# Kernel tuning notes

Hardware: AMD Instinct MI355X
Metric: run time of the kernel (lower is better)

Reference implementation:

```python
import jax, jax.numpy as jnp
import numpy as np

L, B, T, SA, ST = 6, 32, 256, 512, 128
D, H, HD, DFF, OUT = 1024, 16, 64, 4096, 3
ROPE_THETA = 10000.0

def setup_inputs() -> dict:
    key = jax.random.key(0)
    ks = jax.random.split(key, 24)
    w = lambda k, shape: jax.random.normal(k, shape, jnp.float32) * 0.02
    inp = {
        'x':    jax.random.normal(ks[0], (B, T, D), jnp.float32),
        'cond': jax.random.normal(ks[1], (B, D), jnp.float32),
        'adp':  jax.random.normal(ks[2], (B, SA, D), jnp.float32),
        'task': jax.random.normal(ks[3], (B, ST, D), jnp.float32),
        'Wq':  w(ks[4], (L, D, D)),  'bq': jnp.zeros((L, D)),
        'Wks': w(ks[5], (L, D, D)),  'Wvs': w(ks[6], (L, D, D)),
        'Wka': w(ks[7], (L, D, D)),  'Wva': w(ks[8], (L, D, D)),
        'Wkt': w(ks[9], (L, D, D)),  'Wvt': w(ks[10], (L, D, D)),
        'Wo':  w(ks[11], (L, D, D)), 'bo': jnp.zeros((L, D)),
        'qnw': jnp.ones((L, HD)),    'knw': jnp.ones((L, HD)),
        'gate': jnp.zeros((L,)),
        'Wada': w(ks[12], (L, D, 6 * D)), 'bada': jnp.zeros((L, 6 * D)),
        'W1': w(ks[13], (L, D, DFF)), 'b1': jnp.zeros((L, DFF)),
        'W2': w(ks[14], (L, DFF, D)), 'b2': jnp.zeros((L, D)),
        'lnf_w': jnp.ones((D,)), 'lnf_b': jnp.zeros((D,)),
        'Wout': w(ks[15], (D, OUT)), 'bout': jnp.zeros((OUT,)),
    }
    return inp

def _ln(x, eps=1e-5):
    m = x.mean(-1, keepdims=True)
    v = ((x - m) ** 2).mean(-1, keepdims=True)
    return (x - m) * jax.lax.rsqrt(v + eps)

def _rms(x, wgt, eps=1e-6):
    return x * jax.lax.rsqrt((x * x).mean(-1, keepdims=True) + eps) * wgt

def _rotate_half(x):
    h = x.shape[-1] // 2
    return jnp.concatenate([-x[..., h:], x[..., :h]], axis=-1)

def _rope(x, cos, sin):
    # x: (B,S,H,HD); cos/sin: (S,1,HD)
    return x * cos + _rotate_half(x) * sin

def _cos_sin(S):
    inv = 1.0 / (ROPE_THETA ** (jnp.arange(0, HD, 2, dtype=jnp.float32) / HD))
    f = jnp.arange(S, dtype=jnp.float32)[:, None] * inv[None, :]
    emb = jnp.concatenate([f, f], axis=-1)  # (S, HD)
    return jnp.cos(emb)[:, None, :], jnp.sin(emb)[:, None, :]

def _forward(x, cond, adp, task, Wq, bq, Wks, Wvs, Wka, Wva, Wkt, Wvt, Wo, bo,
             qnw, knw, gate, Wada, bada, W1, b1, W2, b2, lnf_w, lnf_b, Wout, bout):
    cosT, sinT = _cos_sin(T)
    cosA, sinA = _cos_sin(SA)
    cosK, sinK = _cos_sin(ST)
    scale = 1.0 / jnp.sqrt(jnp.float32(HD))
    heads = lambda t, W: (t @ W).reshape(t.shape[0], t.shape[1], H, HD)
    for i in range(L):
        ada = jax.nn.silu(cond) @ Wada[i] + bada[i]
        s1, sc1, g1, s2, sc2, g2 = jnp.split(ada, 6, axis=-1)  # each (B,D)
        h = _ln(x) * (1.0 + sc1[:, None]) + s1[:, None]
        # self source: RoPE on Q and K; cross sources: RoPE on K only
        q = _rope(_rms(heads(h, Wq[i]) + bq[i].reshape(H, HD), qnw[i]), cosT, sinT)
        k_s = _rope(_rms(heads(h, Wks[i]), knw[i]), cosT, sinT)
        v_s = heads(h, Wvs[i])
        k_a = _rope(_rms(heads(adp, Wka[i]), knw[i]), cosA, sinA)
        v_a = heads(adp, Wva[i])
        k_t = _rope(_rms(heads(task, Wkt[i]), knw[i]), cosK, sinK)
        v_t = heads(task, Wvt[i])
        ss = jnp.einsum('bthd,bshd->bhts', q, k_s) * scale
        sa = jnp.einsum('bthd,bshd->bhts', q, k_a) * scale
        st = jnp.einsum('bthd,bshd->bhts', q, k_t) * scale * jax.nn.sigmoid(gate[i])
        attn = jax.nn.softmax(jnp.concatenate([ss, sa, st], axis=-1), axis=-1)
        v = jnp.concatenate([v_s, v_a, v_t], axis=1)  # (B, T+SA+ST, H, HD)
        o = jnp.einsum('bhts,bshd->bthd', attn, v).reshape(x.shape[0], T, D)
        x = x + g1[:, None] * (o @ Wo[i] + bo[i])
        h2 = _ln(x) * (1.0 + sc2[:, None]) + s2[:, None]
        ff = jax.nn.gelu(h2 @ W1[i] + b1[i]) @ W2[i] + b2[i]
        x = x + g2[:, None] * ff
    y = _ln(x) * lnf_w + lnf_b
    return y @ Wout + bout

def reference(x, cond, adp, task, Wq, bq, Wks, Wvs, Wka, Wva, Wkt, Wvt, Wo, bo,
              qnw, knw, gate, Wada, bada, W1, b1, W2, b2, lnf_w, lnf_b, Wout, bout):
    return _forward(x, cond, adp, task, Wq, bq, Wks, Wvs, Wka, Wva, Wkt, Wvt, Wo, bo,
                    qnw, knw, gate, Wada, bada, W1, b1, W2, b2, lnf_w, lnf_b, Wout, bout)
```

## Files before the change

kernel.cpp:

```cpp
#include <hip/hip_runtime.h>
#include <stdint.h>

#define DEV static __device__ __forceinline__

#define BB 32
#define TT 256
#define SAA 512
#define STT 128
#define DD 1024
#define HH 16
#define HDD 64
#define DFFF 4096
#define SS 896
#define LL 6

using bf16x8 = __attribute__((ext_vector_type(8))) short;
using f32x4  = __attribute__((ext_vector_type(4))) float;

DEV uint16_t f2bf(float f){
  uint32_t u = __float_as_uint(f);
  uint32_t r = (u + 0x7fffu + ((u >> 16) & 1u)) >> 16;
  return (uint16_t)r;
}
DEV float bf2f(uint16_t b){ return __uint_as_float(((uint32_t)b) << 16); }

typedef __attribute__((address_space(3))) void lds_vt;
typedef __attribute__((address_space(1))) void glb_vt;

DEV void gl_lds16(const uint16_t* g, uint16_t* l){
  __builtin_amdgcn_global_load_lds((const glb_vt*)g, (lds_vt*)l, 16, 0, 0);
}

struct GemmP {
  const uint16_t* A; const uint16_t* B; const uint16_t* B1; const uint16_t* B2;
  uint16_t* outB; float* outF; const float* bias; const float* gvec;
  const float* gatep; float* xres;
  long aOuter, aInner, bOuter, bInner;
  int M, N, K, lda, ldb, ldc, segStart, bShift;
};

template<int MODE>
__global__ __launch_bounds__(256, 2)
void gemm_nt(GemmP p){
  __shared__ uint16_t As[8192];
  __shared__ uint16_t Bs[8192];
  const int tid = threadIdx.x;
  const int w = tid >> 6, l = tid & 63;
  const int n0 = blockIdx.x * 128, m0 = blockIdx.y * 128;
  const int z = blockIdx.z;

  const uint16_t* Ab;
  const uint16_t* Bb;
  if (MODE == 3){
    Ab = p.A + (long)(z >> 4) * p.aOuter + (long)(z & 15) * p.aInner;
    const uint16_t* src; long bo; int nl;
    if (n0 < 256)      { src = p.B;  bo = (long)(z >> 4) * (256 * 1024); nl = n0; }
    else if (n0 < 768) { src = p.B1; bo = (long)(z >> 4) * (512 * 1024); nl = n0 - 256; }
    else               { src = p.B2; bo = (long)(z >> 4) * (128 * 1024); nl = n0 - 768; }
    Bb = src + bo + (long)(z & 15) * 64 + (long)nl * p.ldb;
  } else if (MODE == 4){
    Ab = p.A + (long)z * p.aOuter;
    Bb = p.B + (long)(z >> 4) * p.bOuter + (long)(z & 15) * p.bInner + (long)n0 * p.ldb;
  } else {
    Ab = p.A;
    Bb = p.B + (long)n0 * p.ldb;
  }

  const int rloc = l >> 3, ps = l & 7;
  const int kg_st = (ps - rloc) & 7;

  f32x4 acc[4][4];
  const f32x4 z4 = {0.f, 0.f, 0.f, 0.f};
  #pragma unroll
  for (int a = 0; a < 4; ++a)
    #pragma unroll
    for (int b = 0; b < 4; ++b) acc[a][b] = z4;

  const int KT = p.K >> 6;
  for (int kt = 0; kt < KT; ++kt){
    if (kt) __syncthreads();
    const long kbase = ((long)kt << 6) + (kg_st << 3);
    #pragma unroll
    for (int i = 0; i < 4; ++i){
      const int c = (w << 2) + i;
      int ar = m0 + (c << 3) + rloc;
      if (ar >= p.M) ar = p.M - 1;
      gl_lds16(Ab + (long)ar * p.lda + kbase, &As[c << 9]);
      const int br = (c << 3) + rloc;
      gl_lds16(Bb + (long)br * p.ldb + kbase, &Bs[c << 9]);
    }
    __syncthreads();
    #pragma unroll
    for (int ks = 0; ks < 2; ++ks){
      bf16x8 af[4], bfr[4];
      const int kq = (ks << 2) + (l >> 4);
      #pragma unroll
      for (int mt = 0; mt < 4; ++mt){
        const int r = ((w & 1) << 6) + (mt << 4) + (l & 15);
        af[mt] = *(const bf16x8*)&As[(r << 6) + (((kq + r) & 7) << 3)];
      }
      #pragma unroll
      for (int nt = 0; nt < 4; ++nt){
        const int r = ((w >> 1) << 6) + (nt << 4) + (l & 15);
        bfr[nt] = *(const bf16x8*)&Bs[(r << 6) + (((kq + r) & 7) << 3)];
      }
      #pragma unroll
      for (int mt = 0; mt < 4; ++mt)
        #pragma unroll
        for (int nt = 0; nt < 4; ++nt)
          acc[mt][nt] = __builtin_amdgcn_mfma_f32_16x16x32_bf16(af[mt], bfr[nt], acc[mt][nt], 0, 0, 0);
    }
  }

  float gs = 0.f;
  if (MODE == 3){ float gv = *p.gatep; gs = 0.125f / (1.f + expf(-gv)); }
  const int colb = ((w >> 1) << 6) + (l & 15);
  const int rowb = m0 + ((w & 1) << 6) + ((l >> 4) << 2);
  #pragma unroll
  for (int mt = 0; mt < 4; ++mt){
    #pragma unroll
    for (int nt = 0; nt < 4; ++nt){
      const int col = n0 + colb + (nt << 4);
      const int row0 = rowb + (mt << 4);
      if (MODE == 6){
        const int b = row0 >> p.bShift;
        const int s = row0 & ((1 << p.bShift) - 1);
        const int hh = col >> 6, d = col & 63;
        ushort4 hv;
        hv.x = f2bf(acc[mt][nt][0]); hv.y = f2bf(acc[mt][nt][1]);
        hv.z = f2bf(acc[mt][nt][2]); hv.w = f2bf(acc[mt][nt][3]);
        *(ushort4*)(p.outB + ((long)((b << 4) + hh) * 128 + d) * 896 + p.segStart + s) = hv;
        continue;
      }
      #pragma unroll
      for (int e = 0; e < 4; ++e){
        const int row = row0 + e;
        if (row >= p.M) continue;
        float v = acc[mt][nt][e];
        if (MODE == 0){
          if (p.bias) v += p.bias[col];
          p.outB[(long)row * p.ldc + col] = f2bf(v);
        } else if (MODE == 5){
          v += p.bias[col];
          p.outF[(long)row * p.ldc + col] = v;
        } else if (MODE == 1){
          v += p.bias[col];
          const int b = row >> 8;
          const float g = p.gvec[b * 6144 + col];
          p.xres[(long)row * 1024 + col] += g * v;
        } else if (MODE == 2){
          v += p.bias[col];
          const float u = 0.7978845608028654f * (v + 0.044715f * v * v * v);
          v = 0.5f * v * (1.f + tanhf(u));
          p.outB[(long)row * 4096 + col] = f2bf(v);
        } else if (MODE == 3){
          const float sc = (col >= 768) ? gs : 0.125f;
          p.outF[(long)z * 229376 + (long)row * 896 + col] = v * sc;
        } else if (MODE == 4){
          if (col < 64){
            const int bl = z >> 4, hh = z & 15;
            p.outB[((long)((p.segStart + bl) * 256 + row)) * 1024 + (hh << 6) + col] = f2bf(v);
          }
        }
      }
    }
  }
}

struct WtP { const float* src[11]; uint16_t* dst; };

__global__ __launch_bounds__(256) void k_wtrans(WtP p){
  __shared__ uint16_t tile[64][65];
  const int idx = blockIdx.x, tid = threadIdx.x;
  const int tx = tid & 63, ty = tid >> 6;
  int wi, Kw, Nw, k0, n0;
  if (idx < 2048){ wi = idx >> 8; int t = idx & 255; Kw = 1024; Nw = 1024; k0 = (t >> 4) << 6; n0 = (t & 15) << 6; }
  else if (idx < 3072){ wi = 8; int t = idx - 2048; Kw = 1024; Nw = 4096; k0 = (t >> 6) << 6; n0 = (t & 63) << 6; }
  else if (idx < 4096){ wi = 9; int t = idx - 3072; Kw = 4096; Nw = 1024; k0 = (t >> 4) << 6; n0 = (t & 15) << 6; }
  else { wi = 10; int t = idx - 4096; Kw = 1024; Nw = 6144; k0 = (t / 96) << 6; n0 = (t % 96) << 6; }
  long doff;
  if (wi < 8) doff = (long)wi * 1048576;
  else if (wi == 8) doff = 8388608;
  else if (wi == 9) doff = 12582912;
  else doff = 16777216;
  const float* src = p.src[wi];
  uint16_t* dst = p.dst + doff;
  #pragma unroll 4
  for (int i = 0; i < 16; ++i){
    const int row = (i << 2) + ty;
    tile[row][tx] = f2bf(src[(long)(k0 + row) * Nw + n0 + tx]);
  }
  __syncthreads();
  #pragma unroll 4
  for (int i = 0; i < 16; ++i){
    const int row = (i << 2) + ty;
    dst[(long)(n0 + row) * Kw + k0 + tx] = tile[tx][row];
  }
}

__global__ __launch_bounds__(256) void k_f2bf4(const float* __restrict__ s, uint16_t* __restrict__ d, int n4){
  const int i = blockIdx.x * 256 + threadIdx.x;
  if (i < n4){
    const float4 v = ((const float4*)s)[i];
    ushort4 o; o.x = f2bf(v.x); o.y = f2bf(v.y); o.z = f2bf(v.z); o.w = f2bf(v.w);
    ((ushort4*)d)[i] = o;
  }
}

__global__ __launch_bounds__(256) void k_silu4(const float* __restrict__ s, uint16_t* __restrict__ d, int n4){
  const int i = blockIdx.x * 256 + threadIdx.x;
  if (i < n4){
    const float4 v = ((const float4*)s)[i];
    ushort4 o;
    o.x = f2bf(v.x / (1.f + expf(-v.x)));
    o.y = f2bf(v.y / (1.f + expf(-v.y)));
    o.z = f2bf(v.z / (1.f + expf(-v.z)));
    o.w = f2bf(v.w / (1.f + expf(-v.w)));
    ((ushort4*)d)[i] = o;
  }
}

__global__ __launch_bounds__(256) void k_ln(const float* __restrict__ x,
    const float* __restrict__ addv, const float* __restrict__ mulv,
    uint16_t* __restrict__ outb){
  const int row = blockIdx.x, tid = threadIdx.x;
  const float4 xv = ((const float4*)(x + (long)row * 1024))[tid];
  float s = xv.x + xv.y + xv.z + xv.w;
  float q = xv.x*xv.x + xv.y*xv.y + xv.z*xv.z + xv.w*xv.w;
  #pragma unroll
  for (int o = 32; o; o >>= 1){ s += __shfl_down(s, o); q += __shfl_down(q, o); }
  __shared__ float rs[4], rq[4];
  if ((tid & 63) == 0){ rs[tid >> 6] = s; rq[tid >> 6] = q; }
  __syncthreads();
  s = rs[0] + rs[1] + rs[2] + rs[3];
  q = rq[0] + rq[1] + rq[2] + rq[3];
  const float mean = s * (1.f / 1024.f);
  const float var  = q * (1.f / 1024.f) - mean * mean;
  const float inv  = rsqrtf(var + 1e-5f);
  const int b = row >> 8;
  const float4 av = ((const float4*)(addv + (long)b * 6144))[tid];
  const float4 mv = ((const float4*)(mulv + (long)b * 6144))[tid];
  ushort4 o4;
  o4.x = f2bf((xv.x - mean) * inv * (1.f + mv.x) + av.x);
  o4.y = f2bf((xv.y - mean) * inv * (1.f + mv.y) + av.y);
  o4.z = f2bf((xv.z - mean) * inv * (1.f + mv.z) + av.z);
  o4.w = f2bf((xv.w - mean) * inv * (1.f + mv.w) + av.w);
  ((ushort4*)(outb + (long)row * 1024))[tid] = o4;
}

__global__ __launch_bounds__(256) void k_rmsrope(uint16_t* qb, uint16_t* ksb,
    uint16_t* kab, uint16_t* ktb, const float* qn, const float* kn){
  const int row = blockIdx.x, tid = threadIdx.x;
  const int l = tid & 63, wv = tid >> 6;
  uint16_t* buf; const float* wgt; int pos; long grow;
  if (row < 8192)      { buf = qb;  wgt = qn; grow = row;         pos = row & 255; }
  else if (row < 16384){ buf = ksb; wgt = kn; grow = row - 8192;  pos = (int)grow & 255; }
  else if (row < 32768){ buf = kab; wgt = kn; grow = row - 16384; pos = (int)grow & 511; }
  else                 { buf = ktb; wgt = kn; grow = row - 32768; pos = (int)grow & 127; }
  const float wl = wgt[l];
  const float invf = exp2f(-0.41524101186092029f * (float)(l & 31));
  float c, sn; sincosf((float)pos * invf, &sn, &c);
  const float sgn = (l < 32) ? -1.f : 1.f;
  uint16_t* rbase = buf + grow * 1024;
  #pragma unroll
  for (int hh = 0; hh < 4; ++hh){
    uint16_t* hp = rbase + (((hh << 2) + wv) << 6);
    const float v = bf2f(hp[l]);
    float ss = v * v;
    #pragma unroll
    for (int o = 1; o < 64; o <<= 1) ss += __shfl_xor(ss, o);
    const float y = v * rsqrtf(ss * (1.f / 64.f) + 1e-6f) * wl;
    const float prt = __shfl_xor(y, 32);
    hp[l] = f2bf(y * c + sgn * prt * sn);
  }
}

__global__ __launch_bounds__(256) void k_softmax(const float* __restrict__ sc,
    uint16_t* __restrict__ pr){
  const long row = blockIdx.x;
  const int tid = threadIdx.x, l = tid & 63, w = tid >> 6;
  const float* srow = sc + row * 896;
  float vals[4];
  float mx = -1e30f;
  #pragma unroll
  for (int it = 0; it < 4; ++it){
    const int j = tid + it * 256;
    if (j < 896){ vals[it] = srow[j]; mx = fmaxf(mx, vals[it]); }
  }
  #pragma unroll
  for (int o = 32; o; o >>= 1) mx = fmaxf(mx, __shfl_xor(mx, o));
  __shared__ float red[4];
  if (l == 0) red[w] = mx;
  __syncthreads();
  mx = fmaxf(fmaxf(red[0], red[1]), fmaxf(red[2], red[3]));
  __syncthreads();
  float sum = 0.f;
  #pragma unroll
  for (int it = 0; it < 4; ++it){
    const int j = tid + it * 256;
    if (j < 896){ vals[it] = expf(vals[it] - mx); sum += vals[it]; }
  }
  #pragma unroll
  for (int o = 32; o; o >>= 1) sum += __shfl_xor(sum, o);
  if (l == 0) red[w] = sum;
  __syncthreads();
  const float inv = 1.f / (red[0] + red[1] + red[2] + red[3]);
  uint16_t* prow = pr + row * 896;
  #pragma unroll
  for (int it = 0; it < 4; ++it){
    const int j = tid + it * 256;
    if (j < 896) prow[j] = f2bf(vals[it] * inv);
  }
}

__global__ __launch_bounds__(256) void k_final(const float* __restrict__ x,
    const float* __restrict__ lw, const float* __restrict__ lb,
    const float* __restrict__ W3, const float* __restrict__ b3,
    float* __restrict__ out){
  const int row = blockIdx.x, tid = threadIdx.x;
  const float4 xv = ((const float4*)(x + (long)row * 1024))[tid];
  float s = xv.x + xv.y + xv.z + xv.w;
  float q = xv.x*xv.x + xv.y*xv.y + xv.z*xv.z + xv.w*xv.w;
  #pragma unroll
  for (int o = 32; o; o >>= 1){ s += __shfl_down(s, o); q += __shfl_down(q, o); }
  __shared__ float rs[4], rq[4];
  if ((tid & 63) == 0){ rs[tid >> 6] = s; rq[tid >> 6] = q; }
  __syncthreads();
  s = rs[0] + rs[1] + rs[2] + rs[3];
  q = rq[0] + rq[1] + rq[2] + rq[3];
  const float mean = s * (1.f / 1024.f);
  const float inv  = rsqrtf(q * (1.f / 1024.f) - mean * mean + 1e-5f);
  const float4 wv = ((const float4*)lw)[tid];
  const float4 bv = ((const float4*)lb)[tid];
  const int c = tid << 2;
  const float y0 = (xv.x - mean) * inv * wv.x + bv.x;
  const float y1 = (xv.y - mean) * inv * wv.y + bv.y;
  const float y2 = (xv.z - mean) * inv * wv.z + bv.z;
  const float y3 = (xv.w - mean) * inv * wv.w + bv.w;
  float o0 = y0*W3[c*3+0] + y1*W3[(c+1)*3+0] + y2*W3[(c+2)*3+0] + y3*W3[(c+3)*3+0];
  float o1 = y0*W3[c*3+1] + y1*W3[(c+1)*3+1] + y2*W3[(c+2)*3+1] + y3*W3[(c+3)*3+1];
  float o2 = y0*W3[c*3+2] + y1*W3[(c+1)*3+2] + y2*W3[(c+2)*3+2] + y3*W3[(c+3)*3+2];
  #pragma unroll
  for (int o = 32; o; o >>= 1){
    o0 += __shfl_down(o0, o); o1 += __shfl_down(o1, o); o2 += __shfl_down(o2, o);
  }
  __shared__ float r0[4], r1[4], r2[4];
  if ((tid & 63) == 0){ r0[tid>>6] = o0; r1[tid>>6] = o1; r2[tid>>6] = o2; }
  __syncthreads();
  if (tid == 0){
    out[(long)row * 3 + 0] = r0[0]+r0[1]+r0[2]+r0[3] + b3[0];
    out[(long)row * 3 + 1] = r1[0]+r1[1]+r1[2]+r1[3] + b3[1];
    out[(long)row * 3 + 2] = r2[0]+r2[1]+r2[2]+r2[3] + b3[2];
  }
}

extern "C" void kernel_launch(void* const* d_in, const int* in_sizes, int n_in,
                              void* d_out, int out_size, void* d_ws, size_t ws_size,
                              hipStream_t stream){
  (void)in_sizes; (void)n_in; (void)out_size;
  const float* X    = (const float*)d_in[0];
  const float* cond = (const float*)d_in[1];
  const float* adp  = (const float*)d_in[2];
  const float* task = (const float*)d_in[3];
  const float* Wq   = (const float*)d_in[4];
  const float* bq   = (const float*)d_in[5];
  const float* Wks  = (const float*)d_in[6];
  const float* Wvs  = (const float*)d_in[7];
  const float* Wka  = (const float*)d_in[8];
  const float* Wva  = (const float*)d_in[9];
  const float* Wkt  = (const float*)d_in[10];
  const float* Wvt  = (const float*)d_in[11];
  const float* Wo   = (const float*)d_in[12];
  const float* bo   = (const float*)d_in[13];
  const float* qnw  = (const float*)d_in[14];
  const float* knw  = (const float*)d_in[15];
  const float* gate = (const float*)d_in[16];
  const float* Wada = (const float*)d_in[17];
  const float* bada = (const float*)d_in[18];
  const float* W1   = (const float*)d_in[19];
  const float* b1   = (const float*)d_in[20];
  const float* W2   = (const float*)d_in[21];
  const float* b2   = (const float*)d_in[22];
  const float* lnw  = (const float*)d_in[23];
  const float* lnb  = (const float*)d_in[24];
  const float* Wout = (const float*)d_in[25];
  const float* bout = (const float*)d_in[26];
  float* out = (float*)d_out;

  char* base = (char*)d_ws;
  size_t off = 0;
  auto alloc = [&](size_t bytes)->char*{
    char* r = base + off; off += (bytes + 255) & ~(size_t)255; return r;
  };
  float*    x_cur = (float*)   alloc(8192UL * 1024 * 4);
  float*    ada   = (float*)   alloc(32UL * 6144 * 4);
  uint16_t* csilu = (uint16_t*)alloc(32UL * 1024 * 2);
  uint16_t* hb    = (uint16_t*)alloc(8192UL * 1024 * 2);
  uint16_t* qb    = (uint16_t*)alloc(8192UL * 1024 * 2);
  uint16_t* ksb   = (uint16_t*)alloc(8192UL * 1024 * 2);
  uint16_t* kab   = (uint16_t*)alloc(16384UL * 1024 * 2);
  uint16_t* ktb   = (uint16_t*)alloc(4096UL * 1024 * 2);
  uint16_t* adpb  = (uint16_t*)alloc(16384UL * 1024 * 2);
  uint16_t* taskb = (uint16_t*)alloc(4096UL * 1024 * 2);
  uint16_t* vT    = (uint16_t*)alloc(32UL * 16 * 128 * 896 * 2);
  uint16_t* ob    = (uint16_t*)alloc(8192UL * 1024 * 2);
  uint16_t* Wt    = (uint16_t*)alloc(23068672UL * 2);
  const size_t ff1B = 8192UL * 4096 * 2;
  int BC = 8;
  {
    size_t rem = (ws_size > off) ? ws_size - off : 0;
    auto need = [&](int bc){ size_t a = (size_t)bc * 22020096UL; return a > ff1B ? a : ff1B; };
    if (need(8) <= rem) BC = 8; else if (need(4) <= rem) BC = 4; else BC = 2;
  }
  char* big = alloc((size_t)BC * 22020096UL > ff1B ? (size_t)BC * 22020096UL : ff1B);
  float*    scores = (float*)big;
  uint16_t* probs  = (uint16_t*)(big + (size_t)BC * 14680064UL);
  uint16_t* ff1    = (uint16_t*)big;

  hipMemcpyAsync(x_cur, X, 8192UL * 1024 * 4, hipMemcpyDeviceToDevice, stream);
  k_f2bf4<<<16384, 256, 0, stream>>>(adp,  adpb,  4194304);
  k_f2bf4<<<4096,  256, 0, stream>>>(task, taskb, 1048576);
  k_silu4<<<32,    256, 0, stream>>>(cond, csilu, 8192);

  for (int i = 0; i < LL; ++i){
    WtP wp;
    wp.src[0] = Wq  + (long)i * 1048576;
    wp.src[1] = Wks + (long)i * 1048576;
    wp.src[2] = Wvs + (long)i * 1048576;
    wp.src[3] = Wka + (long)i * 1048576;
    wp.src[4] = Wva + (long)i * 1048576;
    wp.src[5] = Wkt + (long)i * 1048576;
    wp.src[6] = Wvt + (long)i * 1048576;
    wp.src[7] = Wo  + (long)i * 1048576;
    wp.src[8] = W1  + (long)i * 4194304;
    wp.src[9] = W2  + (long)i * 4194304;
    wp.src[10]= Wada+ (long)i * 6291456;
    wp.dst = Wt;
    k_wtrans<<<5632, 256, 0, stream>>>(wp);

    GemmP g;
    auto clr = [&](){ g = GemmP{}; g.aOuter=g.aInner=g.bOuter=g.bInner=0; };

    clr();
    g.A = csilu; g.lda = 1024; g.B = Wt + 16777216; g.ldb = 1024;
    g.M = 32; g.N = 6144; g.K = 1024; g.outF = ada; g.bias = bada + (long)i * 6144; g.ldc = 6144;
    gemm_nt<5><<<dim3(48, 1, 1), 256, 0, stream>>>(g);

    k_ln<<<8192, 256, 0, stream>>>(x_cur, ada + 0, ada + 1024, hb);

    clr(); g.A=hb; g.lda=1024; g.B=Wt; g.ldb=1024; g.M=8192; g.N=1024; g.K=1024;
    g.outB=qb; g.bias=bq + (long)i*1024; g.ldc=1024;
    gemm_nt<0><<<dim3(8, 64, 1), 256, 0, stream>>>(g);

    clr(); g.A=hb; g.lda=1024; g.B=Wt+1048576; g.ldb=1024; g.M=8192; g.N=1024; g.K=1024;
    g.outB=ksb; g.bias=nullptr; g.ldc=1024;
    gemm_nt<0><<<dim3(8, 64, 1), 256, 0, stream>>>(g);

    clr(); g.A=hb; g.lda=1024; g.B=Wt+2097152; g.ldb=1024; g.M=8192; g.N=1024; g.K=1024;
    g.outB=vT; g.bShift=8; g.segStart=0;
    gemm_nt<6><<<dim3(8, 64, 1), 256, 0, stream>>>(g);

    clr(); g.A=adpb; g.lda=1024; g.B=Wt+3145728; g.ldb=1024; g.M=16384; g.N=1024; g.K=1024;
    g.outB=kab; g.bias=nullptr; g.ldc=1024;
    gemm_nt<0><<<dim3(8, 128, 1), 256, 0, stream>>>(g);

    clr(); g.A=adpb; g.lda=1024; g.B=Wt+4194304; g.ldb=1024; g.M=16384; g.N=1024; g.K=1024;
    g.outB=vT; g.bShift=9; g.segStart=256;
    gemm_nt<6><<<dim3(8, 128, 1), 256, 0, stream>>>(g);

    clr(); g.A=taskb; g.lda=1024; g.B=Wt+5242880; g.ldb=1024; g.M=4096; g.N=1024; g.K=1024;
    g.outB=ktb; g.bias=nullptr; g.ldc=1024;
    gemm_nt<0><<<dim3(8, 32, 1), 256, 0, stream>>>(g);

    clr(); g.A=taskb; g.lda=1024; g.B=Wt+6291456; g.ldb=1024; g.M=4096; g.N=1024; g.K=1024;
    g.outB=vT; g.bShift=7; g.segStart=768;
    gemm_nt<6><<<dim3(8, 32, 1), 256, 0, stream>>>(g);

    k_rmsrope<<<36864, 256, 0, stream>>>(qb, ksb, kab, ktb,
                                         qnw + (long)i * 64, knw + (long)i * 64);

    for (int b0 = 0; b0 < 32; b0 += BC){
      clr();
      g.A = qb + (long)b0 * 262144; g.lda = 1024; g.aOuter = 262144; g.aInner = 64;
      g.B  = ksb + (long)b0 * 262144;
      g.B1 = kab + (long)b0 * 524288;
      g.B2 = ktb + (long)b0 * 131072;
      g.ldb = 1024; g.M = 256; g.N = 896; g.K = 64;
      g.outF = scores; g.gatep = gate + i;
      gemm_nt<3><<<dim3(7, 2, BC * 16), 256, 0, stream>>>(g);

      k_softmax<<<BC * 4096, 256, 0, stream>>>(scores, probs);

      clr();
      g.A = probs; g.lda = 896; g.aOuter = 229376;
      g.B = vT + (long)b0 * 1835008; g.bOuter = 1835008; g.bInner = 114688;
      g.ldb = 896; g.M = 256; g.N = 128; g.K = 896;
      g.outB = ob; g.segStart = b0;
      gemm_nt<4><<<dim3(1, 2, BC * 16), 256, 0, stream>>>(g);
    }

    clr(); g.A=ob; g.lda=1024; g.B=Wt+7340032; g.ldb=1024; g.M=8192; g.N=1024; g.K=1024;
    g.bias=bo + (long)i*1024; g.gvec=ada + 2048; g.xres=x_cur;
    gemm_nt<1><<<dim3(8, 64, 1), 256, 0, stream>>>(g);

    k_ln<<<8192, 256, 0, stream>>>(x_cur, ada + 3072, ada + 4096, hb);

    clr(); g.A=hb; g.lda=1024; g.B=Wt+8388608; g.ldb=1024; g.M=8192; g.N=4096; g.K=1024;
    g.outB=ff1; g.bias=b1 + (long)i*4096;
    gemm_nt<2><<<dim3(32, 64, 1), 256, 0, stream>>>(g);

    clr(); g.A=ff1; g.lda=4096; g.B=Wt+12582912; g.ldb=4096; g.M=8192; g.N=1024; g.K=4096;
    g.bias=b2 + (long)i*1024; g.gvec=ada + 5120; g.xres=x_cur;
    gemm_nt<1><<<dim3(8, 64, 1), 256, 0, stream>>>(g);
  }

  k_final<<<8192, 256, 0, stream>>>(x_cur, lnw, lnb, Wout, bout, out);
}
```

Before: 7.091 ms.

## Fuse attention scores, softmax and PV into a single flash-attention kernel

Replaces the three-stage attention (score GEMM writing fp32 scores, a separate softmax kernel, then a PV GEMM) with one kernel that uses an online softmax over 64-key tiles and keeps probabilities in LDS. This removes the large fp32 score and bf16 probability round trips through global memory and the batch-chunk loop of launches. In exchange, each block handles one (batch, head) pair with only 512 blocks, and per-tile syncs plus online-softmax rescaling add work inside the kernel.

```diff
diff --git a/kernel.cpp b/kernel.cpp
--- a/kernel.cpp
+++ b/kernel.cpp
@@ -47,24 +47,9 @@
   const int tid = threadIdx.x;
   const int w = tid >> 6, l = tid & 63;
   const int n0 = blockIdx.x * 128, m0 = blockIdx.y * 128;
-  const int z = blockIdx.z;
-
-  const uint16_t* Ab;
-  const uint16_t* Bb;
-  if (MODE == 3){
-    Ab = p.A + (long)(z >> 4) * p.aOuter + (long)(z & 15) * p.aInner;
-    const uint16_t* src; long bo; int nl;
-    if (n0 < 256)      { src = p.B;  bo = (long)(z >> 4) * (256 * 1024); nl = n0; }
-    else if (n0 < 768) { src = p.B1; bo = (long)(z >> 4) * (512 * 1024); nl = n0 - 256; }
-    else               { src = p.B2; bo = (long)(z >> 4) * (128 * 1024); nl = n0 - 768; }
-    Bb = src + bo + (long)(z & 15) * 64 + (long)nl * p.ldb;
-  } else if (MODE == 4){
-    Ab = p.A + (long)z * p.aOuter;
-    Bb = p.B + (long)(z >> 4) * p.bOuter + (long)(z & 15) * p.bInner + (long)n0 * p.ldb;
-  } else {
-    Ab = p.A;
-    Bb = p.B + (long)n0 * p.ldb;
-  }
+
+  const uint16_t* Ab = p.A;
+  const uint16_t* Bb = p.B + (long)n0 * p.ldb;
 
   const int rloc = l >> 3, ps = l & 7;
   const int kg_st = (ps - rloc) & 7;
@@ -112,8 +97,6 @@
     }
   }
 
-  float gs = 0.f;
-  if (MODE == 3){ float gv = *p.gatep; gs = 0.125f / (1.f + expf(-gv)); }
   const int colb = ((w >> 1) << 6) + (l & 15);
   const int rowb = m0 + ((w & 1) << 6) + ((l >> 4) << 2);
   #pragma unroll
@@ -153,17 +136,161 @@
           const float u = 0.7978845608028654f * (v + 0.044715f * v * v * v);
           v = 0.5f * v * (1.f + tanhf(u));
           p.outB[(long)row * 4096 + col] = f2bf(v);
-        } else if (MODE == 3){
-          const float sc = (col >= 768) ? gs : 0.125f;
-          p.outF[(long)z * 229376 + (long)row * 896 + col] = v * sc;
-        } else if (MODE == 4){
-          if (col < 64){
-            const int bl = z >> 4, hh = z & 15;
-            p.outB[((long)((p.segStart + bl) * 256 + row)) * 1024 + (hh << 6) + col] = f2bf(v);
-          }
         }
       }
     }
+  }
+}
+
+__global__ __launch_bounds__(256, 2)
+void k_attn(const uint16_t* __restrict__ qb, const uint16_t* __restrict__ ksb,
+            const uint16_t* __restrict__ kab, const uint16_t* __restrict__ ktb,
+            const uint16_t* __restrict__ vT, uint16_t* __restrict__ ob,
+            const float* __restrict__ gatep){
+  __shared__ uint16_t Kl[4096];
+  __shared__ uint16_t Vl[4096];
+  __shared__ uint16_t Pl[16384];
+  const int tid = threadIdx.x;
+  const int w = tid >> 6, l = tid & 63;
+  const int bh = blockIdx.x, b = bh >> 4, h = bh & 15;
+  const int g = l >> 4, c = l & 15;
+
+  bf16x8 qf[4][2];
+  const uint16_t* qbase = qb + (((long)(b * 256 + w * 64)) << 10) + (h << 6);
+  #pragma unroll
+  for (int m = 0; m < 4; ++m)
+    #pragma unroll
+    for (int ks = 0; ks < 2; ++ks)
+      qf[m][ks] = *(const bf16x8*)(qbase + (((long)(m * 16 + c)) << 10) + ks * 32 + (g << 3));
+
+  f32x4 acc_o[4][4];
+  const f32x4 z4 = {0.f, 0.f, 0.f, 0.f};
+  #pragma unroll
+  for (int m = 0; m < 4; ++m)
+    #pragma unroll
+    for (int n = 0; n < 4; ++n) acc_o[m][n] = z4;
+  float mstate[4][4], lstate[4][4];
+  #pragma unroll
+  for (int m = 0; m < 4; ++m)
+    #pragma unroll
+    for (int r = 0; r < 4; ++r){ mstate[m][r] = -1e30f; lstate[m][r] = 0.f; }
+
+  const float gv = *gatep;
+  const float gs = 0.125f / (1.f + __expf(-gv));
+  uint16_t* pw = Pl + (w << 12);
+
+  for (int kt = 0; kt < 14; ++kt){
+    if (kt) __syncthreads();
+    #pragma unroll
+    for (int j = 0; j < 2; ++j){
+      const int rr = (w << 4) + (j << 3) + (l >> 3);
+      const int s = (kt << 6) + rr;
+      const uint16_t* src; long row;
+      if (s < 256){ src = ksb; row = (long)b * 256 + s; }
+      else if (s < 768){ src = kab; row = (long)b * 512 + (s - 256); }
+      else { src = ktb; row = (long)b * 128 + (s - 768); }
+      const int blk = (l & 7) ^ (rr & 7);
+      gl_lds16(src + (row << 10) + (h << 6) + (blk << 3),
+               &Kl[((w << 4) + (j << 3)) << 6]);
+      gl_lds16(vT + (long)(bh * 128 + rr) * 896 + (kt << 6) + (blk << 3),
+               &Vl[((w << 4) + (j << 3)) << 6]);
+    }
+    __syncthreads();
+
+    f32x4 sacc[4][4];
+    #pragma unroll
+    for (int m = 0; m < 4; ++m)
+      #pragma unroll
+      for (int n = 0; n < 4; ++n) sacc[m][n] = z4;
+    #pragma unroll
+    for (int ks = 0; ks < 2; ++ks){
+      bf16x8 kf[4];
+      #pragma unroll
+      for (int n = 0; n < 4; ++n){
+        const int s = (n << 4) + c;
+        const int blk = (ks << 2) + g;
+        kf[n] = *(const bf16x8*)&Kl[(s << 6) + ((blk ^ (s & 7)) << 3)];
+      }
+      #pragma unroll
+      for (int m = 0; m < 4; ++m)
+        #pragma unroll
+        for (int n = 0; n < 4; ++n)
+          sacc[m][n] = __builtin_amdgcn_mfma_f32_16x16x32_bf16(qf[m][ks], kf[n], sacc[m][n], 0, 0, 0);
+    }
+
+    const float tsc = (kt >= 12) ? gs : 0.125f;
+    #pragma unroll
+    for (int m = 0; m < 4; ++m){
+      float nm[4], corr[4], tsum[4];
+      #pragma unroll
+      for (int r = 0; r < 4; ++r){
+        float t = fmaxf(fmaxf(sacc[m][0][r], sacc[m][1][r]),
+                        fmaxf(sacc[m][2][r], sacc[m][3][r])) * tsc;
+        #pragma unroll
+        for (int o = 1; o < 16; o <<= 1) t = fmaxf(t, __shfl_xor(t, o));
+        nm[r] = fmaxf(mstate[m][r], t);
+        corr[r] = __expf(mstate[m][r] - nm[r]);
+        mstate[m][r] = nm[r];
+        tsum[r] = 0.f;
+      }
+      const int q4 = (m << 4) + (g << 2);
+      #pragma unroll
+      for (int n = 0; n < 4; ++n){
+        #pragma unroll
+        for (int r = 0; r < 4; ++r){
+          const float p = __expf(sacc[m][n][r] * tsc - nm[r]);
+          tsum[r] += p;
+          const int q = q4 + r;
+          const int s = (n << 4) + c;
+          pw[(q << 6) + (((s >> 3) ^ (q & 7)) << 3) + (s & 7)] = f2bf(p);
+        }
+      }
+      #pragma unroll
+      for (int r = 0; r < 4; ++r){
+        float t = tsum[r];
+        #pragma unroll
+        for (int o = 1; o < 16; o <<= 1) t += __shfl_xor(t, o);
+        lstate[m][r] = lstate[m][r] * corr[r] + t;
+        #pragma unroll
+        for (int n = 0; n < 4; ++n) acc_o[m][n][r] *= corr[r];
+      }
+    }
+
+    #pragma unroll
+    for (int ks = 0; ks < 2; ++ks){
+      bf16x8 pf[4], vf[4];
+      #pragma unroll
+      for (int m = 0; m < 4; ++m){
+        const int q = (m << 4) + c;
+        const int blk = (ks << 2) + g;
+        pf[m] = *(const bf16x8*)&pw[(q << 6) + ((blk ^ (q & 7)) << 3)];
+      }
+      #pragma unroll
+      for (int n = 0; n < 4; ++n){
+        const int d = (n << 4) + c;
+        const int blk = (ks << 2) + g;
+        vf[n] = *(const bf16x8*)&Vl[(d << 6) + ((blk ^ (d & 7)) << 3)];
+      }
+      #pragma unroll
+      for (int m = 0; m < 4; ++m)
+        #pragma unroll
+        for (int n = 0; n < 4; ++n)
+          acc_o[m][n] = __builtin_amdgcn_mfma_f32_16x16x32_bf16(pf[m], vf[n], acc_o[m][n], 0, 0, 0);
+    }
+  }
+
+  uint16_t* obase = ob + (((long)(b * 256 + w * 64)) << 10) + (h << 6);
+  #pragma unroll
+  for (int m = 0; m < 4; ++m){
+    float inv[4];
+    #pragma unroll
+    for (int r = 0; r < 4; ++r) inv[r] = 1.f / lstate[m][r];
+    #pragma unroll
+    for (int n = 0; n < 4; ++n)
+      #pragma unroll
+      for (int r = 0; r < 4; ++r)
+        obase[(((long)((m << 4) + (g << 2) + r)) << 10) + (n << 4) + c] =
+            f2bf(acc_o[m][n][r] * inv[r]);
   }
 }
 
@@ -275,44 +402,6 @@
   }
 }
 
-__global__ __launch_bounds__(256) void k_softmax(const float* __restrict__ sc,
-    uint16_t* __restrict__ pr){
-  const long row = blockIdx.x;
-  const int tid = threadIdx.x, l = tid & 63, w = tid >> 6;
-  const float* srow = sc + row * 896;
-  float vals[4];
-  float mx = -1e30f;
-  #pragma unroll
-  for (int it = 0; it < 4; ++it){
-    const int j = tid + it * 256;
-    if (j < 896){ vals[it] = srow[j]; mx = fmaxf(mx, vals[it]); }
-  }
-  #pragma unroll
-  for (int o = 32; o; o >>= 1) mx = fmaxf(mx, __shfl_xor(mx, o));
-  __shared__ float red[4];
-  if (l == 0) red[w] = mx;
-  __syncthreads();
-  mx = fmaxf(fmaxf(red[0], red[1]), fmaxf(red[2], red[3]));
-  __syncthreads();
-  float sum = 0.f;
-  #pragma unroll
-  for (int it = 0; it < 4; ++it){
-    const int j = tid + it * 256;
-    if (j < 896){ vals[it] = expf(vals[it] - mx); sum += vals[it]; }
-  }
-  #pragma unroll
-  for (int o = 32; o; o >>= 1) sum += __shfl_xor(sum, o);
-  if (l == 0) red[w] = sum;
-  __syncthreads();
-  const float inv = 1.f / (red[0] + red[1] + red[2] + red[3]);
-  uint16_t* prow = pr + row * 896;
-  #pragma unroll
-  for (int it = 0; it < 4; ++it){
-    const int j = tid + it * 256;
-    if (j < 896) prow[j] = f2bf(vals[it] * inv);
-  }
-}
-
 __global__ __launch_bounds__(256) void k_final(const float* __restrict__ x,
     const float* __restrict__ lw, const float* __restrict__ lb,
     const float* __restrict__ W3, const float* __restrict__ b3,
@@ -357,7 +446,7 @@
 extern "C" void kernel_launch(void* const* d_in, const int* in_sizes, int n_in,
                               void* d_out, int out_size, void* d_ws, size_t ws_size,
                               hipStream_t stream){
-  (void)in_sizes; (void)n_in; (void)out_size;
+  (void)in_sizes; (void)n_in; (void)out_size; (void)ws_size;
   const float* X    = (const float*)d_in[0];
   const float* cond = (const float*)d_in[1];
   const float* adp  = (const float*)d_in[2];
@@ -405,17 +494,7 @@
   uint16_t* vT    = (uint16_t*)alloc(32UL * 16 * 128 * 896 * 2);
   uint16_t* ob    = (uint16_t*)alloc(8192UL * 1024 * 2);
   uint16_t* Wt    = (uint16_t*)alloc(23068672UL * 2);
-  const size_t ff1B = 8192UL * 4096 * 2;
-  int BC = 8;
-  {
-    size_t rem = (ws_size > off) ? ws_size - off : 0;
-    auto need = [&](int bc){ size_t a = (size_t)bc * 22020096UL; return a > ff1B ? a : ff1B; };
-    if (need(8) <= rem) BC = 8; else if (need(4) <= rem) BC = 4; else BC = 2;
-  }
-  char* big = alloc((size_t)BC * 22020096UL > ff1B ? (size_t)BC * 22020096UL : ff1B);
-  float*    scores = (float*)big;
-  uint16_t* probs  = (uint16_t*)(big + (size_t)BC * 14680064UL);
-  uint16_t* ff1    = (uint16_t*)big;
+  uint16_t* ff1   = (uint16_t*)alloc(8192UL * 4096 * 2);
 
   hipMemcpyAsync(x_cur, X, 8192UL * 1024 * 4, hipMemcpyDeviceToDevice, stream);
   k_f2bf4<<<16384, 256, 0, stream>>>(adp,  adpb,  4194304);
@@ -479,25 +558,7 @@
     k_rmsrope<<<36864, 256, 0, stream>>>(qb, ksb, kab, ktb,
                                          qnw + (long)i * 64, knw + (long)i * 64);
 
-    for (int b0 = 0; b0 < 32; b0 += BC){
-      clr();
-      g.A = qb + (long)b0 * 262144; g.lda = 1024; g.aOuter = 262144; g.aInner = 64;
-      g.B  = ksb + (long)b0 * 262144;
-      g.B1 = kab + (long)b0 * 524288;
-      g.B2 = ktb + (long)b0 * 131072;
-      g.ldb = 1024; g.M = 256; g.N = 896; g.K = 64;
-      g.outF = scores; g.gatep = gate + i;
-      gemm_nt<3><<<dim3(7, 2, BC * 16), 256, 0, stream>>>(g);
-
-      k_softmax<<<BC * 4096, 256, 0, stream>>>(scores, probs);
-
-      clr();
-      g.A = probs; g.lda = 896; g.aOuter = 229376;
-      g.B = vT + (long)b0 * 1835008; g.bOuter = 1835008; g.bInner = 114688;
-      g.ldb = 896; g.M = 256; g.N = 128; g.K = 896;
-      g.outB = ob; g.segStart = b0;
-      gemm_nt<4><<<dim3(1, 2, BC * 16), 256, 0, stream>>>(g);
-    }
+    k_attn<<<512, 256, 0, stream>>>(qb, ksb, kab, ktb, vT, ob, gate + i);
 
     clr(); g.A=ob; g.lda=1024; g.B=Wt+7340032; g.ldb=1024; g.M=8192; g.N=1024; g.K=1024;
     g.bias=bo + (long)i*1024; g.gvec=ada + 2048; g.xres=x_cur;
```

Result: faster. 6.592 ms (-7.0%).
